# Optimization experiments

Hardware: AMD Instinct MI355X
Metric: run time of the kernel (lower is better)

## Reference

```python
import math
import jax, jax.numpy as jnp
import numpy as np

HEAD_SIZE = 64
MAX_LEN = 1024
ENT_HEADS = 2
REL_HEADS = 24
NEG_BIG = 1e12


def rope_tables(max_pos=MAX_LEN, head_size=HEAD_SIZE):
    # coord_dim=2 -> table built with d_hid = head_size // 2
    d = head_size // 2
    pos = jnp.arange(max_pos, dtype=jnp.float32)[:, None]            # [P,1]
    div = jnp.exp(jnp.arange(0, d, 2, dtype=jnp.float32) * (-math.log(10000.0) / d))  # [d/2]
    ang = pos * div                                                   # [P, d/2]
    # table[:,1::2]=cos, table[:,::2]=sin; repeat_interleave(2) == jnp.repeat(...,2)
    cosp = jnp.repeat(jnp.cos(ang), 2, axis=-1)                       # [P, d]
    sinp = jnp.repeat(jnp.sin(ang), 2, axis=-1)                       # [P, d]
    return cosp, sinp


def apply_rope2d(qw, cosp, sinp, xp, yp):
    # qw: [b,s,h,hs]; xp,yp: [b,s] int positions
    cos = jnp.concatenate([cosp[xp], cosp[yp]], axis=-1)[:, :, None, :]  # [b,s,1,hs]
    sin = jnp.concatenate([sinp[xp], sinp[yp]], axis=-1)[:, :, None, :]
    qw2 = jnp.stack([-qw[..., 1::2], qw[..., ::2]], axis=-1).reshape(qw.shape)
    return qw * cos + qw2 * sin


def gp_layer(x, W, b, heads, mask, xp, yp, cosp, sinp, tril):
    hs = HEAD_SIZE
    bsz, s, _ = x.shape
    # dense then torch.chunk(heads)+stack == reshape to [b,s,heads,2*hs]
    seq = (x @ W + b).reshape(bsz, s, heads, 2 * hs)
    qw, kw = seq[..., :hs], seq[..., hs:]
    qw = apply_rope2d(qw, cosp, sinp, xp, yp)
    kw = apply_rope2d(kw, cosp, sinp, xp, yp)
    logits = jnp.einsum('bmhd,bnhd->bhmn', qw, kw)                    # [b,h,s,s]
    pad = (mask[:, None, :, None] > 0) & (mask[:, None, None, :] > 0)
    logits = jnp.where(pad, logits, -jnp.inf)
    if tril:
        logits = logits - jnp.tril(jnp.ones((s, s), logits.dtype), -1) * NEG_BIG
    return logits / (hs ** 0.5)


def setup_inputs() -> dict:
    key = jax.random.key(0)
    ks = jax.random.split(key, 8)
    b, s, h = 4, 512, 1024
    return {
        'last_hidden_state': jax.random.normal(ks[0], (b, s, h), dtype=jnp.float32),
        'attention_mask': jnp.ones((b, s), dtype=jnp.int32),
        'x_pos': jax.random.randint(ks[1], (b, s), 0, MAX_LEN, dtype=jnp.int32),
        'y_pos': jax.random.randint(ks[2], (b, s), 0, MAX_LEN, dtype=jnp.int32),
        'W_ent': jax.random.normal(ks[3], (h, ENT_HEADS * 2 * HEAD_SIZE), dtype=jnp.float32) * 0.02,
        'b_ent': jnp.zeros((ENT_HEADS * 2 * HEAD_SIZE,), dtype=jnp.float32),
        'W_head': jax.random.normal(ks[4], (h, REL_HEADS * 2 * HEAD_SIZE), dtype=jnp.float32) * 0.02,
        'b_head': jnp.zeros((REL_HEADS * 2 * HEAD_SIZE,), dtype=jnp.float32),
        'W_tail': jax.random.normal(ks[5], (h, REL_HEADS * 2 * HEAD_SIZE), dtype=jnp.float32) * 0.02,
        'b_tail': jnp.zeros((REL_HEADS * 2 * HEAD_SIZE,), dtype=jnp.float32),
    }


def reference(last_hidden_state, attention_mask, x_pos, y_pos,
              W_ent, b_ent, W_head, b_head, W_tail, b_tail):
    cosp, sinp = rope_tables()
    ent = gp_layer(last_hidden_state, W_ent, b_ent, ENT_HEADS,
                   attention_mask, x_pos, y_pos, cosp, sinp, tril=True)
    head = gp_layer(last_hidden_state, W_head, b_head, REL_HEADS,
                    attention_mask, x_pos, y_pos, cosp, sinp, tril=False)
    tail = gp_layer(last_hidden_state, W_tail, b_tail, REL_HEADS,
                    attention_mask, x_pos, y_pos, cosp, sinp, tril=False)
    return jnp.concatenate([ent, head, tail], axis=1)  # [b, 2+24+24, s, s]
```

## Files before the change

kernel.cpp:

```cpp
#include <hip/hip_runtime.h>
#include <hip/hip_bf16.h>
#include <math.h>

#define NUM_B 4
#define SEQ 512
#define HID 1024
#define NH 50
#define NCOL 6400
#define M_TOK 2048

typedef short bf16x8_t __attribute__((ext_vector_type(8)));
typedef float f32x4_t __attribute__((ext_vector_type(4)));

__device__ __forceinline__ unsigned short f2bf(float f) {
    union { float f; unsigned int u; } v; v.f = f;
    unsigned int u = v.u;
    u += 0x7fffu + ((u >> 16) & 1u);
    return (unsigned short)(u >> 16);
}

__device__ __forceinline__ void gload_lds16(const void* g, void* l) {
    __builtin_amdgcn_global_load_lds(
        (__attribute__((address_space(1))) unsigned int*)(unsigned long long)g,
        (__attribute__((address_space(3))) unsigned int*)(unsigned long long)(uintptr_t)l,
        16, 0, 0);
}

__global__ void k_prep(const float* __restrict__ x, unsigned short* __restrict__ xb,
                       float2* __restrict__ csT,
                       const float* __restrict__ be, const float* __restrict__ bh,
                       const float* __restrict__ bt, float* __restrict__ ball) {
    int bid = blockIdx.x, tid = threadIdx.x;
    if (bid < 2048) {
        int i = bid * 256 + tid;
        float4 v = ((const float4*)x)[i];
        ushort4 o;
        o.x = f2bf(v.x); o.y = f2bf(v.y); o.z = f2bf(v.z); o.w = f2bf(v.w);
        ((ushort4*)xb)[i] = o;
    } else if (bid < 2112) {
        int idx = (bid - 2048) * 256 + tid;
        int p = idx >> 4, t2 = idx & 15;
        float ang = (float)p * expf(-logf(10000.f) * (float)(2 * t2) / 32.f);
        csT[idx] = make_float2(cosf(ang), sinf(ang));
    } else {
        int i = (bid - 2112) * 256 + tid;
        if (i < 6400) {
            float v;
            if (i < 256) v = be[i];
            else if (i < 3328) v = bh[i - 256];
            else v = bt[i - 3328];
            ball[i] = v;
        }
    }
}

__global__ void k_cvt_w(const float* __restrict__ We, const float* __restrict__ Wh,
                        const float* __restrict__ Wl, unsigned short* __restrict__ Wo) {
    __shared__ float t[32][33];
    int n = blockIdx.x * 32 + threadIdx.x;
    const float* W; int Nw, nc;
    if (n < 256)       { W = We; Nw = 256;  nc = n; }
    else if (n < 3328) { W = Wh; Nw = 3072; nc = n - 256; }
    else               { W = Wl; Nw = 3072; nc = n - 3328; }
    int k = blockIdx.y * 32 + threadIdx.y;
    t[threadIdx.y][threadIdx.x] = W[(size_t)k * Nw + nc];
    __syncthreads();
    int on = blockIdx.x * 32 + threadIdx.y;
    int ok = blockIdx.y * 32 + threadIdx.x;
    Wo[(size_t)on * HID + ok] = f2bf(t[threadIdx.x][threadIdx.y]);
}

__global__ __launch_bounds__(256) void k_gemm1(const unsigned short* __restrict__ A,
                                               const unsigned short* __restrict__ Bt,
                                               const float* __restrict__ bias,
                                               const int* __restrict__ xp,
                                               const int* __restrict__ yp,
                                               const float2* __restrict__ csT,
                                               unsigned short* __restrict__ seq) {
    __shared__ __align__(16) unsigned short As[128 * 64];
    __shared__ __align__(16) unsigned short Bs[128 * 64];
    int tid = threadIdx.x;
    int wave = tid >> 6, lane = tid & 63;
    int l15 = lane & 15, q = lane >> 4;
    int m0 = blockIdx.x * 128, n0 = blockIdx.y * 128;
    int wm = (wave >> 1) * 64, wn = (wave & 1) * 64;

    f32x4_t acc[4][4];
#pragma unroll
    for (int i = 0; i < 4; i++)
#pragma unroll
        for (int j = 0; j < 4; j++) acc[i][j] = (f32x4_t){0.f, 0.f, 0.f, 0.f};

    for (int k0 = 0; k0 < HID; k0 += 64) {
        __syncthreads();
#pragma unroll
        for (int it = 0; it < 4; ++it) {
            int c = it * 256 + tid;
            int r = c >> 3, cl = c & 7;
            int cg = cl ^ (r & 7);
            gload_lds16(A + (size_t)(m0 + r) * HID + k0 + cg * 8, As + c * 8);
            gload_lds16(Bt + (size_t)(n0 + r) * HID + k0 + cg * 8, Bs + c * 8);
        }
        __syncthreads();
#pragma unroll
        for (int ks = 0; ks < 2; ++ks) {
            bf16x8_t af[4], bfr[4];
#pragma unroll
            for (int i = 0; i < 4; i++) {
                int r = wm + i * 16 + l15;
                int cl = (ks * 4 + q) ^ (r & 7);
                af[i] = *(const bf16x8_t*)&As[r * 64 + cl * 8];
            }
#pragma unroll
            for (int j = 0; j < 4; j++) {
                int r = wn + j * 16 + l15;
                int cl = (ks * 4 + q) ^ (r & 7);
                bfr[j] = *(const bf16x8_t*)&Bs[r * 64 + cl * 8];
            }
#pragma unroll
            for (int i = 0; i < 4; i++)
#pragma unroll
                for (int j = 0; j < 4; j++)
                    acc[i][j] = __builtin_amdgcn_mfma_f32_16x16x32_bf16(bfr[j], af[i], acc[i][j], 0, 0, 0);
        }
    }

    float4 bj[4];
#pragma unroll
    for (int j = 0; j < 4; j++)
        bj[j] = *(const float4*)&bias[n0 + wn + j * 16 + q * 4];
#pragma unroll
    for (int i = 0; i < 4; i++) {
        int m = m0 + wm + i * 16 + l15;
        int posx = xp[m] * 16, posy = yp[m] * 16;
#pragma unroll
        for (int j = 0; j < 4; j++) {
            float v0 = acc[i][j][0] + bj[j].x;
            float v1 = acc[i][j][1] + bj[j].y;
            float v2 = acc[i][j][2] + bj[j].z;
            float v3 = acc[i][j][3] + bj[j].w;
            int pos = (j < 2) ? posx : posy;
            int t2 = (j & 1) * 8 + q * 2;
            float2 cs0 = csT[pos + t2];
            float2 cs1 = csT[pos + t2 + 1];
            float r0 = v0 * cs0.x - v1 * cs0.y;
            float r1 = v1 * cs0.x + v0 * cs0.y;
            float r2 = v2 * cs1.x - v3 * cs1.y;
            float r3 = v3 * cs1.x + v2 * cs1.y;
            ushort4 o;
            o.x = f2bf(r0); o.y = f2bf(r1); o.z = f2bf(r2); o.w = f2bf(r3);
            *(ushort4*)&seq[(size_t)m * NCOL + n0 + wn + j * 16 + q * 4] = o;
        }
    }
}

__global__ __launch_bounds__(256) void k_attn(const unsigned short* __restrict__ seq,
                                              const int* __restrict__ mask,
                                              float* __restrict__ out) {
    __shared__ __align__(16) unsigned short Qs[128 * 64];
    __shared__ __align__(16) unsigned short Ks[128 * 64];
    int tid = threadIdx.x;
    int bh = blockIdx.z;
    int b = bh / NH, h = bh - b * NH;
    int m0 = blockIdx.x * 128, n0 = blockIdx.y * 128;
    const unsigned short* qbase = seq + (size_t)b * SEQ * NCOL + h * 128;

#pragma unroll
    for (int it = 0; it < 4; ++it) {
        int c = it * 256 + tid;
        int r = c >> 3, cl = c & 7;
        int cg = cl ^ (r & 7);
        gload_lds16(qbase + (size_t)(m0 + r) * NCOL + cg * 8, Qs + c * 8);
        gload_lds16(qbase + (size_t)(n0 + r) * NCOL + 64 + cg * 8, Ks + c * 8);
    }
    __syncthreads();

    int wave = tid >> 6, lane = tid & 63;
    int l15 = lane & 15, q = lane >> 4;
    int wm = (wave >> 1) * 64, wn = (wave & 1) * 64;

    f32x4_t acc[4][4];
#pragma unroll
    for (int i = 0; i < 4; i++)
#pragma unroll
        for (int j = 0; j < 4; j++) acc[i][j] = (f32x4_t){0.f, 0.f, 0.f, 0.f};

#pragma unroll
    for (int ks = 0; ks < 2; ++ks) {
        bf16x8_t af[4], bfr[4];
#pragma unroll
        for (int i = 0; i < 4; i++) {
            int r = wm + i * 16 + l15;
            int cl = (ks * 4 + q) ^ (r & 7);
            af[i] = *(const bf16x8_t*)&Qs[r * 64 + cl * 8];
        }
#pragma unroll
        for (int j = 0; j < 4; j++) {
            int r = wn + j * 16 + l15;
            int cl = (ks * 4 + q) ^ (r & 7);
            bfr[j] = *(const bf16x8_t*)&Ks[r * 64 + cl * 8];
        }
#pragma unroll
        for (int i = 0; i < 4; i++)
#pragma unroll
            for (int j = 0; j < 4; j++)
                acc[i][j] = __builtin_amdgcn_mfma_f32_16x16x32_bf16(bfr[j], af[i], acc[i][j], 0, 0, 0);
    }

    const int* mrow = mask + b * SEQ;
    bool ent = (h < 2);
    size_t obase = (size_t)bh * SEQ * SEQ;
    int4 mn[4];
#pragma unroll
    for (int j = 0; j < 4; j++)
        mn[j] = *(const int4*)&mrow[n0 + wn + j * 16 + q * 4];
#pragma unroll
    for (int i = 0; i < 4; i++) {
        int m = m0 + wm + i * 16 + l15;
        bool mz = (mrow[m] == 0);
#pragma unroll
        for (int j = 0; j < 4; j++) {
            int nb = n0 + wn + j * 16 + q * 4;
            float4 v;
            v.x = acc[i][j][0] * 0.125f;
            v.y = acc[i][j][1] * 0.125f;
            v.z = acc[i][j][2] * 0.125f;
            v.w = acc[i][j][3] * 0.125f;
            if (ent) {
                if (m > nb)     v.x -= 1.25e11f;
                if (m > nb + 1) v.y -= 1.25e11f;
                if (m > nb + 2) v.z -= 1.25e11f;
                if (m > nb + 3) v.w -= 1.25e11f;
            }
            if (mz || mn[j].x == 0) v.x = -INFINITY;
            if (mz || mn[j].y == 0) v.y = -INFINITY;
            if (mz || mn[j].z == 0) v.z = -INFINITY;
            if (mz || mn[j].w == 0) v.w = -INFINITY;
            *(float4*)&out[obase + (size_t)m * SEQ + nb] = v;
        }
    }
}

extern "C" void kernel_launch(void* const* d_in, const int* in_sizes, int n_in,
                              void* d_out, int out_size, void* d_ws, size_t ws_size,
                              hipStream_t stream) {
    const float* x      = (const float*)d_in[0];
    const int*   mask   = (const int*)d_in[1];
    const int*   xp     = (const int*)d_in[2];
    const int*   yp     = (const int*)d_in[3];
    const float* W_ent  = (const float*)d_in[4];
    const float* b_ent  = (const float*)d_in[5];
    const float* W_head = (const float*)d_in[6];
    const float* b_head = (const float*)d_in[7];
    const float* W_tail = (const float*)d_in[8];
    const float* b_tail = (const float*)d_in[9];
    float* out = (float*)d_out;

    char* ws = (char*)d_ws;
    size_t off = 0;
    auto alloc = [&](size_t bytes) {
        void* p = ws + off;
        off += (bytes + 255) & ~(size_t)255;
        return p;
    };
    float2* csT = (float2*)alloc(16384 * 8);
    unsigned short* xb  = (unsigned short*)alloc((size_t)M_TOK * HID * 2);
    unsigned short* Wt  = (unsigned short*)alloc((size_t)NCOL * HID * 2);
    float* ball = (float*)alloc(NCOL * 4);
    unsigned short* seq = (unsigned short*)alloc((size_t)M_TOK * NCOL * 2);

    k_prep<<<2137, 256, 0, stream>>>(x, xb, csT, b_ent, b_head, b_tail, ball);
    k_cvt_w<<<dim3(200, 32), dim3(32, 32), 0, stream>>>(W_ent, W_head, W_tail, Wt);
    k_gemm1<<<dim3(16, 50), 256, 0, stream>>>(xb, Wt, ball, xp, yp, csT, seq);
    k_attn<<<dim3(4, 4, 200), 256, 0, stream>>>(seq, mask, out);
}
```

Before: 328.9 us.

## Fuse projection GEMM with RoPE and QK^T into one per-head kernel

Replaces the separate projection GEMM and attention-logit kernels with one kernel per (batch, head). Each block computes the 512x128 projected Q/K tile, applies bias and RoPE, and stages the result as bf16 in shared memory. It then computes QK^T from LDS and writes the masked, scaled logits. This removes the global write and re-read of the intermediate seq buffer and one launch. The cost is a grid of only 200 large blocks using 144KB of dynamic LDS each, which limits occupancy and leaves some CUs idle, with no overlap between the GEMM loads and compute.

```diff
diff --git a/kernel.cpp b/kernel.cpp
--- a/kernel.cpp
+++ b/kernel.cpp
@@ -70,69 +70,92 @@
     Wo[(size_t)on * HID + ok] = f2bf(t[threadIdx.x][threadIdx.y]);
 }
 
-__global__ __launch_bounds__(256) void k_gemm1(const unsigned short* __restrict__ A,
-                                               const unsigned short* __restrict__ Bt,
-                                               const float* __restrict__ bias,
-                                               const int* __restrict__ xp,
-                                               const int* __restrict__ yp,
-                                               const float2* __restrict__ csT,
-                                               unsigned short* __restrict__ seq) {
-    __shared__ __align__(16) unsigned short As[128 * 64];
-    __shared__ __align__(16) unsigned short Bs[128 * 64];
+#define FUSED_LDS_BYTES (144 * 1024)
+
+__global__ __launch_bounds__(512, 2) void k_fused(const unsigned short* __restrict__ xb,
+                                                  const unsigned short* __restrict__ Wt,
+                                                  const float* __restrict__ bias,
+                                                  const int* __restrict__ xp,
+                                                  const int* __restrict__ yp,
+                                                  const float2* __restrict__ csT,
+                                                  const int* __restrict__ mask,
+                                                  float* __restrict__ out) {
+    extern __shared__ unsigned short smem[];
+    unsigned short* As = smem;
+    unsigned short* Bs = smem + 512 * 64;
+    unsigned short* Qs = smem;
+    unsigned short* Ks = smem + 640 * 64;
+
     int tid = threadIdx.x;
     int wave = tid >> 6, lane = tid & 63;
     int l15 = lane & 15, q = lane >> 4;
-    int m0 = blockIdx.x * 128, n0 = blockIdx.y * 128;
-    int wm = (wave >> 1) * 64, wn = (wave & 1) * 64;
-
-    f32x4_t acc[4][4];
-#pragma unroll
-    for (int i = 0; i < 4; i++)
+    int bh = blockIdx.x;
+    int b = bh / NH, h = bh - b * NH;
+
+    const unsigned short* Ab = xb + (size_t)b * SEQ * HID;
+    const unsigned short* Bb = Wt + (size_t)h * 128 * HID;
+
+    f32x4_t acc[8][4];
+#pragma unroll
+    for (int i = 0; i < 8; i++)
 #pragma unroll
         for (int j = 0; j < 4; j++) acc[i][j] = (f32x4_t){0.f, 0.f, 0.f, 0.f};
+
+    int wmg = (wave >> 1) * 128;
+    int wqk = wave & 1;
 
     for (int k0 = 0; k0 < HID; k0 += 64) {
         __syncthreads();
 #pragma unroll
-        for (int it = 0; it < 4; ++it) {
-            int c = it * 256 + tid;
+        for (int it = 0; it < 8; ++it) {
+            int c = it * 512 + tid;
             int r = c >> 3, cl = c & 7;
             int cg = cl ^ (r & 7);
-            gload_lds16(A + (size_t)(m0 + r) * HID + k0 + cg * 8, As + c * 8);
-            gload_lds16(Bt + (size_t)(n0 + r) * HID + k0 + cg * 8, Bs + c * 8);
+            gload_lds16(Ab + (size_t)r * HID + k0 + cg * 8, As + c * 8);
+        }
+#pragma unroll
+        for (int it = 0; it < 2; ++it) {
+            int c = it * 512 + tid;
+            int r = c >> 3, cl = c & 7;
+            int cg = cl ^ (r & 7);
+            gload_lds16(Bb + (size_t)r * HID + k0 + cg * 8, Bs + c * 8);
         }
         __syncthreads();
 #pragma unroll
         for (int ks = 0; ks < 2; ++ks) {
-            bf16x8_t af[4], bfr[4];
-#pragma unroll
-            for (int i = 0; i < 4; i++) {
-                int r = wm + i * 16 + l15;
+            bf16x8_t af[8], bfr[4];
+#pragma unroll
+            for (int i = 0; i < 8; i++) {
+                int r = wmg + i * 16 + l15;
                 int cl = (ks * 4 + q) ^ (r & 7);
                 af[i] = *(const bf16x8_t*)&As[r * 64 + cl * 8];
             }
 #pragma unroll
             for (int j = 0; j < 4; j++) {
-                int r = wn + j * 16 + l15;
+                int r = wqk * 64 + j * 16 + l15;
                 int cl = (ks * 4 + q) ^ (r & 7);
                 bfr[j] = *(const bf16x8_t*)&Bs[r * 64 + cl * 8];
             }
 #pragma unroll
-            for (int i = 0; i < 4; i++)
+            for (int i = 0; i < 8; i++)
 #pragma unroll
                 for (int j = 0; j < 4; j++)
                     acc[i][j] = __builtin_amdgcn_mfma_f32_16x16x32_bf16(bfr[j], af[i], acc[i][j], 0, 0, 0);
         }
     }
 
+    __syncthreads();
+
     float4 bj[4];
 #pragma unroll
     for (int j = 0; j < 4; j++)
-        bj[j] = *(const float4*)&bias[n0 + wn + j * 16 + q * 4];
-#pragma unroll
-    for (int i = 0; i < 4; i++) {
-        int m = m0 + wm + i * 16 + l15;
-        int posx = xp[m] * 16, posy = yp[m] * 16;
+        bj[j] = *(const float4*)&bias[h * 128 + wqk * 64 + j * 16 + q * 4];
+    unsigned short* dst = wqk ? Ks : Qs;
+#pragma unroll
+    for (int i = 0; i < 8; i++) {
+        int m = wmg + i * 16 + l15;
+        int mg = b * SEQ + m;
+        int posx = xp[mg] * 16, posy = yp[mg] * 16;
 #pragma unroll
         for (int j = 0; j < 4; j++) {
             float v0 = acc[i][j][0] + bj[j].x;
@@ -149,94 +172,85 @@
             float r3 = v3 * cs1.x + v2 * cs1.y;
             ushort4 o;
             o.x = f2bf(r0); o.y = f2bf(r1); o.z = f2bf(r2); o.w = f2bf(r3);
-            *(ushort4*)&seq[(size_t)m * NCOL + n0 + wn + j * 16 + q * 4] = o;
-        }
-    }
-}
-
-__global__ __launch_bounds__(256) void k_attn(const unsigned short* __restrict__ seq,
-                                              const int* __restrict__ mask,
-                                              float* __restrict__ out) {
-    __shared__ __align__(16) unsigned short Qs[128 * 64];
-    __shared__ __align__(16) unsigned short Ks[128 * 64];
-    int tid = threadIdx.x;
-    int bh = blockIdx.z;
-    int b = bh / NH, h = bh - b * NH;
-    int m0 = blockIdx.x * 128, n0 = blockIdx.y * 128;
-    const unsigned short* qbase = seq + (size_t)b * SEQ * NCOL + h * 128;
-
-#pragma unroll
-    for (int it = 0; it < 4; ++it) {
-        int c = it * 256 + tid;
-        int r = c >> 3, cl = c & 7;
-        int cg = cl ^ (r & 7);
-        gload_lds16(qbase + (size_t)(m0 + r) * NCOL + cg * 8, Qs + c * 8);
-        gload_lds16(qbase + (size_t)(n0 + r) * NCOL + 64 + cg * 8, Ks + c * 8);
+            int cl0 = j * 2 + (q >> 1);
+            int swz = cl0 ^ (m & 7);
+            *(ushort4*)&dst[m * 64 + swz * 8 + (q & 1) * 4] = o;
+        }
     }
     __syncthreads();
 
-    int wave = tid >> 6, lane = tid & 63;
-    int l15 = lane & 15, q = lane >> 4;
-    int wm = (wave >> 1) * 64, wn = (wave & 1) * 64;
-
-    f32x4_t acc[4][4];
-#pragma unroll
-    for (int i = 0; i < 4; i++)
-#pragma unroll
-        for (int j = 0; j < 4; j++) acc[i][j] = (f32x4_t){0.f, 0.f, 0.f, 0.f};
-
-#pragma unroll
-    for (int ks = 0; ks < 2; ++ks) {
-        bf16x8_t af[4], bfr[4];
+    bf16x8_t qf[4][2];
+#pragma unroll
+    for (int i = 0; i < 4; i++) {
+        int r = wave * 64 + i * 16 + l15;
+#pragma unroll
+        for (int ks = 0; ks < 2; ks++) {
+            int cl = (ks * 4 + q) ^ (r & 7);
+            qf[i][ks] = *(const bf16x8_t*)&Qs[r * 64 + cl * 8];
+        }
+    }
+
+    const int* mrow = mask + b * SEQ;
+    bool enth = (h < 2);
+    size_t obase = (size_t)bh * SEQ * SEQ;
+    int mloc[4]; bool mz[4];
+#pragma unroll
+    for (int i = 0; i < 4; i++) {
+        mloc[i] = wave * 64 + i * 16 + l15;
+        mz[i] = (mrow[mloc[i]] == 0);
+    }
+
+    for (int nc = 0; nc < 8; ++nc) {
+        bf16x8_t kf[4][2];
+#pragma unroll
+        for (int j = 0; j < 4; j++) {
+            int r = nc * 64 + j * 16 + l15;
+#pragma unroll
+            for (int ks = 0; ks < 2; ks++) {
+                int cl = (ks * 4 + q) ^ (r & 7);
+                kf[j][ks] = *(const bf16x8_t*)&Ks[r * 64 + cl * 8];
+            }
+        }
+        f32x4_t a2[4][4];
+#pragma unroll
+        for (int i = 0; i < 4; i++)
+#pragma unroll
+            for (int j = 0; j < 4; j++) a2[i][j] = (f32x4_t){0.f, 0.f, 0.f, 0.f};
+#pragma unroll
+        for (int ks = 0; ks < 2; ks++)
+#pragma unroll
+            for (int i = 0; i < 4; i++)
+#pragma unroll
+                for (int j = 0; j < 4; j++)
+                    a2[i][j] = __builtin_amdgcn_mfma_f32_16x16x32_bf16(kf[j][ks], qf[i][ks], a2[i][j], 0, 0, 0);
+
+        int4 mn[4];
+#pragma unroll
+        for (int j = 0; j < 4; j++)
+            mn[j] = *(const int4*)&mrow[nc * 64 + j * 16 + q * 4];
 #pragma unroll
         for (int i = 0; i < 4; i++) {
-            int r = wm + i * 16 + l15;
-            int cl = (ks * 4 + q) ^ (r & 7);
-            af[i] = *(const bf16x8_t*)&Qs[r * 64 + cl * 8];
-        }
-#pragma unroll
-        for (int j = 0; j < 4; j++) {
-            int r = wn + j * 16 + l15;
-            int cl = (ks * 4 + q) ^ (r & 7);
-            bfr[j] = *(const bf16x8_t*)&Ks[r * 64 + cl * 8];
-        }
-#pragma unroll
-        for (int i = 0; i < 4; i++)
-#pragma unroll
-            for (int j = 0; j < 4; j++)
-                acc[i][j] = __builtin_amdgcn_mfma_f32_16x16x32_bf16(bfr[j], af[i], acc[i][j], 0, 0, 0);
-    }
-
-    const int* mrow = mask + b * SEQ;
-    bool ent = (h < 2);
-    size_t obase = (size_t)bh * SEQ * SEQ;
-    int4 mn[4];
-#pragma unroll
-    for (int j = 0; j < 4; j++)
-        mn[j] = *(const int4*)&mrow[n0 + wn + j * 16 + q * 4];
-#pragma unroll
-    for (int i = 0; i < 4; i++) {
-        int m = m0 + wm + i * 16 + l15;
-        bool mz = (mrow[m] == 0);
-#pragma unroll
-        for (int j = 0; j < 4; j++) {
-            int nb = n0 + wn + j * 16 + q * 4;
-            float4 v;
-            v.x = acc[i][j][0] * 0.125f;
-            v.y = acc[i][j][1] * 0.125f;
-            v.z = acc[i][j][2] * 0.125f;
-            v.w = acc[i][j][3] * 0.125f;
-            if (ent) {
-                if (m > nb)     v.x -= 1.25e11f;
-                if (m > nb + 1) v.y -= 1.25e11f;
-                if (m > nb + 2) v.z -= 1.25e11f;
-                if (m > nb + 3) v.w -= 1.25e11f;
-            }
-            if (mz || mn[j].x == 0) v.x = -INFINITY;
-            if (mz || mn[j].y == 0) v.y = -INFINITY;
-            if (mz || mn[j].z == 0) v.z = -INFINITY;
-            if (mz || mn[j].w == 0) v.w = -INFINITY;
-            *(float4*)&out[obase + (size_t)m * SEQ + nb] = v;
+            int m = mloc[i];
+#pragma unroll
+            for (int j = 0; j < 4; j++) {
+                int nb = nc * 64 + j * 16 + q * 4;
+                float4 v;
+                v.x = a2[i][j][0] * 0.125f;
+                v.y = a2[i][j][1] * 0.125f;
+                v.z = a2[i][j][2] * 0.125f;
+                v.w = a2[i][j][3] * 0.125f;
+                if (enth) {
+                    if (m > nb)     v.x -= 1.25e11f;
+                    if (m > nb + 1) v.y -= 1.25e11f;
+                    if (m > nb + 2) v.z -= 1.25e11f;
+                    if (m > nb + 3) v.w -= 1.25e11f;
+                }
+                if (mz[i] || mn[j].x == 0) v.x = -INFINITY;
+                if (mz[i] || mn[j].y == 0) v.y = -INFINITY;
+                if (mz[i] || mn[j].z == 0) v.z = -INFINITY;
+                if (mz[i] || mn[j].w == 0) v.w = -INFINITY;
+                *(float4*)&out[obase + (size_t)m * SEQ + nb] = v;
+            }
         }
     }
 }
@@ -267,10 +281,16 @@
     unsigned short* xb  = (unsigned short*)alloc((size_t)M_TOK * HID * 2);
     unsigned short* Wt  = (unsigned short*)alloc((size_t)NCOL * HID * 2);
     float* ball = (float*)alloc(NCOL * 4);
-    unsigned short* seq = (unsigned short*)alloc((size_t)M_TOK * NCOL * 2);
+
+    static bool attr_done = false;
+    if (!attr_done) {
+        (void)hipFuncSetAttribute((const void*)k_fused,
+                                  hipFuncAttributeMaxDynamicSharedMemorySize,
+                                  FUSED_LDS_BYTES);
+        attr_done = true;
+    }
 
     k_prep<<<2137, 256, 0, stream>>>(x, xb, csT, b_ent, b_head, b_tail, ball);
     k_cvt_w<<<dim3(200, 32), dim3(32, 32), 0, stream>>>(W_ent, W_head, W_tail, Wt);
-    k_gemm1<<<dim3(16, 50), 256, 0, stream>>>(xb, Wt, ball, xp, yp, csT, seq);
-    k_attn<<<dim3(4, 4, 200), 256, 0, stream>>>(seq, mask, out);
-}
+    k_fused<<<NUM_B * NH, 512, FUSED_LDS_BYTES, stream>>>(xb, Wt, ball, xp, yp, csT, mask, out);
+}
```

Result: faster. 308.0 us (-6.4%).
